# Performance work log

Hardware: AMD Instinct MI355X
Metric: run time of the kernel (lower is better)

Reference implementation:

```python
import jax, jax.numpy as jnp
import numpy as np

MAX_BITS = 256.0  # 2**8


def _quantize_kernel(kern):
    # ConfigurableDense.quantize(): symmetric 8-bit fake-quantization of the kernel.
    # qmin starts at 1e10, qmax at -1e10, so first call uses min/max of kernel.
    qmin = jnp.minimum(jnp.float32(1e10), jnp.min(kern))
    qmax = jnp.maximum(jnp.float32(-1e10), jnp.max(kern))
    s = 2.0 * jnp.maximum(jnp.abs(qmin), jnp.abs(qmax)) / MAX_BITS
    return jnp.round(kern / s) * s


def setup_inputs() -> dict:
    key = jax.random.key(0)
    ks = jax.random.split(key, 9)
    B, S, D_IN, D_MODEL = 4, 2048, 1024, 1024
    sc = 0.02
    return {
        "q": jax.random.normal(ks[0], (B, S, D_IN), jnp.float32),
        "k": jax.random.normal(ks[1], (B, S, D_IN), jnp.float32),
        "v": jax.random.normal(ks[2], (B, S, D_IN), jnp.float32),
        "Wq": jax.random.normal(ks[3], (D_IN, D_MODEL), jnp.float32) * sc,
        "bq": jax.random.normal(ks[4], (D_MODEL,), jnp.float32) * sc,
        "Wk": jax.random.normal(ks[5], (D_IN, D_MODEL), jnp.float32) * sc,
        "bk": jax.random.normal(ks[6], (D_MODEL,), jnp.float32) * sc,
        "Wv": jax.random.normal(ks[7], (D_IN, D_MODEL), jnp.float32) * sc,
        "bv": jax.random.normal(ks[8], (D_MODEL,), jnp.float32) * sc,
    }


def reference(q, k, v, Wq, bq, Wk, bk, Wv, bv):
    # Projections with fake-quantized kernels (ConfigurableDense, activation=None).
    qp = jnp.einsum('bsi,id->bsd', q, _quantize_kernel(Wq)) + bq
    kp = jnp.einsum('bsi,id->bsd', k, _quantize_kernel(Wk)) + bk
    vp = jnp.einsum('bsi,id->bsd', v, _quantize_kernel(Wv)) + bv
    # MovingAverageQuantizers are identity on the first call (steps=0 < warmup).
    dk = jnp.float32(kp.shape[-1])
    logits = jnp.einsum('bqd,bkd->bqk', qp, kp) / jnp.sqrt(dk)  # [B, S, S]
    attn = jax.nn.softmax(logits, axis=-1)
    return jnp.einsum('bqk,bkd->bqd', attn, vp)
```

## Files before the change

kernel.cpp:

```cpp
#include <hip/hip_runtime.h>
#include <stdint.h>


typedef unsigned short ushort_t;
typedef __attribute__((ext_vector_type(8))) short short8;
typedef __bf16 bf16x8 __attribute__((ext_vector_type(8)));
typedef __attribute__((ext_vector_type(4))) float floatx4;
typedef __attribute__((ext_vector_type(8))) int int8v;

__device__ __forceinline__ ushort_t f2bf(float x) {
  unsigned u = __float_as_uint(x);
  unsigned r = (u + 0x7fffu + ((u >> 16) & 1u)) >> 16;
  return (ushort_t)r;
}
__device__ __forceinline__ float bf2f(ushort_t u) {
  return __uint_as_float(((unsigned)u) << 16);
}
__device__ __forceinline__ unsigned char f2fp8(float x) {
  return (unsigned char)(__builtin_amdgcn_cvt_pk_fp8_f32(x, x, 0, false) & 0xff);
}
__device__ __forceinline__ int cvtpk_bf16(float a, float b) {
  unsigned r;
  asm("v_cvt_pk_bf16_f32 %0, %1, %2" : "=v"(r) : "v"(a), "v"(b));
  return (int)r;
}

__device__ __forceinline__ void gl_lds16(const void* g, void* l) {
  __builtin_amdgcn_global_load_lds(
      (const __attribute__((address_space(1))) unsigned int*)g,
      (__attribute__((address_space(3))) unsigned int*)l, 16, 0, 0);
}

__global__ __launch_bounds__(256, 2) void proj_f32a(
    const float* __restrict__ Aq, const float* __restrict__ Ak,
    const float* __restrict__ Av, const ushort_t* __restrict__ Bt,
    void* __restrict__ Cv, void* __restrict__ Cv8,
    const float* __restrict__ bias0, const float* __restrict__ bias1,
    const float* __restrict__ bias2) {
  __shared__ __attribute__((aligned(16))) ushort_t sA[128 * 64];
  __shared__ __attribute__((aligned(16))) ushort_t sB[128 * 64];

  const int t = threadIdx.x;
  const int lane = t & 63;
  const int wave = t >> 6;
  const int bm = blockIdx.x;
  const int bn = blockIdx.y;
  const int bz = blockIdx.z;

  const float* Ab = bz == 0 ? Aq : (bz == 1 ? Ak : Av);
  const ushort_t* Bb = Bt + (long)bz * 1048576L;

  const long a_row0 = (long)bm * 128;
  const long b_row0 = (long)bn * 128;

  const int crow = t >> 3;
  const int schunk = (t & 7) ^ (crow & 7);
  const ushort_t* gB = Bb + (b_row0 + crow) * 1024 + schunk * 8;
  ushort_t* lB = sB + wave * 512;

  const int arow = t >> 3;
  const int achk = t & 7;
  const float* gA = Ab + (a_row0 + arow) * 1024 + achk * 8;
  int awr[4];
#pragma unroll
  for (int k = 0; k < 4; ++k)
    awr[k] = (k * 32 + arow) * 64 + ((achk ^ (arow & 7)) * 8);

  floatx4 acc[4][4];
#pragma unroll
  for (int i = 0; i < 4; ++i)
#pragma unroll
    for (int j = 0; j < 4; ++j) acc[i][j] = {0.f, 0.f, 0.f, 0.f};

  const int wm = (wave & 1) * 64;
  const int wn = (wave >> 1) * 64;
  const int fr = lane & 15;
  const int fg = lane >> 4;

  int offA[2][4], offB[2][4];
#pragma unroll
  for (int s = 0; s < 2; ++s)
#pragma unroll
    for (int i = 0; i < 4; ++i) {
      int rowA = wm + i * 16 + fr;
      int rowB = wn + i * 16 + fr;
      int cg = s * 4 + fg;
      offA[s][i] = rowA * 64 + ((cg ^ (rowA & 7)) * 8);
      offB[s][i] = rowB * 64 + ((cg ^ (rowB & 7)) * 8);
    }

  float4 aL[8];
#pragma unroll
  for (int k = 0; k < 4; ++k) {
    aL[2 * k] = *(const float4*)(gA + (long)k * 32 * 1024);
    aL[2 * k + 1] = *(const float4*)(gA + (long)k * 32 * 1024 + 4);
  }

#pragma unroll 1
  for (int k0 = 0; k0 < 1024; k0 += 64) {
#pragma unroll
    for (int k = 0; k < 4; ++k) {
      int4 w;
      w.x = cvtpk_bf16(aL[2 * k].x, aL[2 * k].y);
      w.y = cvtpk_bf16(aL[2 * k].z, aL[2 * k].w);
      w.z = cvtpk_bf16(aL[2 * k + 1].x, aL[2 * k + 1].y);
      w.w = cvtpk_bf16(aL[2 * k + 1].z, aL[2 * k + 1].w);
      *(int4*)&sA[awr[k]] = w;
    }
#pragma unroll
    for (int i = 0; i < 4; ++i)
      gl_lds16(gB + (long)i * 32 * 1024 + k0, lB + i * 2048);
    __builtin_amdgcn_sched_barrier(0);
    {
      const long kn = (k0 + 64) & 1023;
#pragma unroll
      for (int k = 0; k < 4; ++k) {
        aL[2 * k] = *(const float4*)(gA + (long)k * 32 * 1024 + kn);
        aL[2 * k + 1] = *(const float4*)(gA + (long)k * 32 * 1024 + kn + 4);
      }
    }
    asm volatile("s_waitcnt lgkmcnt(0) vmcnt(8)" ::: "memory");
    __builtin_amdgcn_sched_barrier(0);
    __builtin_amdgcn_s_barrier();
    __builtin_amdgcn_sched_barrier(0);

#pragma unroll
    for (int s = 0; s < 2; ++s) {
      bf16x8 af[4], bfr[4];
#pragma unroll
      for (int i = 0; i < 4; ++i) {
        af[i] = *(const bf16x8*)&sA[offA[s][i]];
        bfr[i] = *(const bf16x8*)&sB[offB[s][i]];
      }
#pragma unroll
      for (int mi = 0; mi < 4; ++mi)
#pragma unroll
        for (int ni = 0; ni < 4; ++ni)
          acc[mi][ni] = __builtin_amdgcn_mfma_f32_16x16x32_bf16(
              af[mi], bfr[ni], acc[mi][ni], 0, 0, 0);
    }
    __builtin_amdgcn_sched_barrier(0);
    __builtin_amdgcn_s_barrier();
    __builtin_amdgcn_sched_barrier(0);
  }

  const int r0 = fg * 4;
  const int cc = fr;
  const float* bias = bz == 0 ? bias0 : (bz == 1 ? bias1 : bias2);
  unsigned char* C8 = (unsigned char*)Cv8 + (long)bz * 8388608L;
  ushort_t* CvpT = (ushort_t*)Cv;

#pragma unroll
  for (int mi = 0; mi < 4; ++mi) {
#pragma unroll
    for (int ni = 0; ni < 4; ++ni) {
      long gm0 = a_row0 + wm + mi * 16 + r0;
      long gn = b_row0 + wn + ni * 16 + cc;
      float vv[4];
#pragma unroll
      for (int r = 0; r < 4; ++r) vv[r] = acc[mi][ni][r] + bias[gn];
      if (bz == 2) {
        long b = gm0 >> 11, s = gm0 & 2047;
        ushort4 u4;
        u4.x = f2bf(vv[0]);
        u4.y = f2bf(vv[1]);
        u4.z = f2bf(vv[2]);
        u4.w = f2bf(vv[3]);
        *(ushort4*)&CvpT[b * (2048L * 1024L) + gn * 2048L + s] = u4;
      } else {
#pragma unroll
        for (int r = 0; r < 4; ++r) C8[(gm0 + r) * 1024 + gn] = f2fp8(vv[r]);
      }
    }
  }
}

#define BM 128
#define BN 128
#define BK 64

template <int CMODE, int SWAP>
__global__ __launch_bounds__(256, 2) void gemm_bt(
    const ushort_t* __restrict__ A, const ushort_t* __restrict__ Bt,
    void* __restrict__ Cv, void* __restrict__ Cv8,
    const float* __restrict__ bias0, const float* __restrict__ bias1,
    const float* __restrict__ bias2, int K, int ldc, float alpha, long strideA,
    long strideB, long strideC) {
  __shared__ __attribute__((aligned(16))) ushort_t sA[BM * BK];
  __shared__ __attribute__((aligned(16))) ushort_t sB[BN * BK];

  const int t = threadIdx.x;
  const int lane = t & 63;
  const int wave = t >> 6;
  const int bm = SWAP ? blockIdx.x : blockIdx.y;
  const int bn = SWAP ? blockIdx.y : blockIdx.x;
  const int bz = blockIdx.z;

  const ushort_t* Ab = A + (long)bz * strideA;
  const ushort_t* Bb = Bt + (long)bz * strideB;

  const long a_row0 = (long)bm * BM;
  const long b_row0 = (long)bn * BN;

  const int crow = t >> 3;
  const int schunk = (t & 7) ^ (crow & 7);

  const ushort_t* gA = Ab + (a_row0 + crow) * (long)K + schunk * 8;
  const ushort_t* gB = Bb + (b_row0 + crow) * (long)K + schunk * 8;

  ushort_t* lA = sA + wave * 512;
  ushort_t* lB = sB + wave * 512;

  floatx4 acc[4][4];
#pragma unroll
  for (int i = 0; i < 4; ++i)
#pragma unroll
    for (int j = 0; j < 4; ++j) acc[i][j] = {0.f, 0.f, 0.f, 0.f};

  const int wm = (wave & 1) * 64;
  const int wn = (wave >> 1) * 64;
  const int fr = lane & 15;
  const int fg = lane >> 4;

  int offA[2][4], offB[2][4];
#pragma unroll
  for (int s = 0; s < 2; ++s)
#pragma unroll
    for (int i = 0; i < 4; ++i) {
      int rowA = wm + i * 16 + fr;
      int rowB = wn + i * 16 + fr;
      int cg = s * 4 + fg;
      offA[s][i] = rowA * BK + ((cg ^ (rowA & 7)) * 8);
      offB[s][i] = rowB * BK + ((cg ^ (rowB & 7)) * 8);
    }

  for (int k0 = 0; k0 < K; k0 += BK) {
#pragma unroll
    for (int i = 0; i < 4; ++i) {
      gl_lds16(gA + (long)i * 32 * K, lA + i * 2048);
      gl_lds16(gB + (long)i * 32 * K, lB + i * 2048);
    }
    gA += BK;
    gB += BK;
    __syncthreads();

#pragma unroll
    for (int s = 0; s < 2; ++s) {
      bf16x8 af[4], bfr[4];
#pragma unroll
      for (int i = 0; i < 4; ++i) {
        af[i] = *(const bf16x8*)&sA[offA[s][i]];
        bfr[i] = *(const bf16x8*)&sB[offB[s][i]];
      }
#pragma unroll
      for (int mi = 0; mi < 4; ++mi)
#pragma unroll
        for (int ni = 0; ni < 4; ++ni)
          acc[mi][ni] = __builtin_amdgcn_mfma_f32_16x16x32_bf16(
              af[mi], bfr[ni], acc[mi][ni], 0, 0, 0);
    }
    __syncthreads();
  }

  const int r0 = fg * 4;
  const int cc = fr;
  float* Cz32 = (float*)Cv + (long)bz * strideC;

#pragma unroll
  for (int mi = 0; mi < 4; ++mi) {
#pragma unroll
    for (int ni = 0; ni < 4; ++ni) {
      long gm0 = a_row0 + wm + mi * 16 + r0;
      long gn = b_row0 + wn + ni * 16 + cc;
      float vv[4];
#pragma unroll
      for (int r = 0; r < 4; ++r) vv[r] = acc[mi][ni][r] * alpha;
      if (CMODE == 2) {
#pragma unroll
        for (int r = 0; r < 4; ++r) Cz32[(gm0 + r) * ldc + gn] = vv[r];
      }
    }
  }
}

__global__ __launch_bounds__(256, 2) void qk_fp8(
    const unsigned char* __restrict__ Q8, const unsigned char* __restrict__ K8,
    ushort_t* __restrict__ P) {
  __shared__ __attribute__((aligned(16))) unsigned char sA[128 * 128];
  __shared__ __attribute__((aligned(16))) unsigned char sB[128 * 128];
  const int t = threadIdx.x;
  const int lane = t & 63, wave = t >> 6;
  const int bm = blockIdx.x, bn = blockIdx.y, bz = blockIdx.z;

  const unsigned char* Ab = Q8 + (long)bz * 2097152L + (long)bm * 128 * 1024;
  const unsigned char* Bb = K8 + (long)bz * 2097152L + (long)bn * 128 * 1024;

  const int crow = t >> 3;
  const int schunk = (t & 7) ^ (crow & 7);
  const unsigned char* gA = Ab + crow * 1024 + schunk * 16;
  const unsigned char* gB = Bb + crow * 1024 + schunk * 16;
  unsigned char* lA = sA + wave * 1024;
  unsigned char* lB = sB + wave * 1024;

  floatx4 acc[4][4];
#pragma unroll
  for (int i = 0; i < 4; ++i)
#pragma unroll
    for (int j = 0; j < 4; ++j) acc[i][j] = {0.f, 0.f, 0.f, 0.f};

  const int wm = (wave & 1) * 64;
  const int wn = (wave >> 1) * 64;
  const int fr = lane & 15;
  const int fg = lane >> 4;

  int offA[4][2], offB[4][2];
#pragma unroll
  for (int i = 0; i < 4; ++i) {
    int rA = wm + i * 16 + fr;
    int rB = wn + i * 16 + fr;
    offA[i][0] = rA * 128 + (((2 * fg) ^ (rA & 7)) * 16);
    offA[i][1] = rA * 128 + (((2 * fg + 1) ^ (rA & 7)) * 16);
    offB[i][0] = rB * 128 + (((2 * fg) ^ (rB & 7)) * 16);
    offB[i][1] = rB * 128 + (((2 * fg + 1) ^ (rB & 7)) * 16);
  }

  for (int k0 = 0; k0 < 1024; k0 += 128) {
#pragma unroll
    for (int i = 0; i < 4; ++i) {
      gl_lds16(gA + (long)i * 32 * 1024, lA + i * 4096);
      gl_lds16(gB + (long)i * 32 * 1024, lB + i * 4096);
    }
    gA += 128;
    gB += 128;
    __syncthreads();

    int8v af[4], bfr[4];
#pragma unroll
    for (int i = 0; i < 4; ++i) {
      int4 lo = *(const int4*)&sA[offA[i][0]];
      int4 hi = *(const int4*)&sA[offA[i][1]];
      af[i][0] = lo.x; af[i][1] = lo.y; af[i][2] = lo.z; af[i][3] = lo.w;
      af[i][4] = hi.x; af[i][5] = hi.y; af[i][6] = hi.z; af[i][7] = hi.w;
      int4 lo2 = *(const int4*)&sB[offB[i][0]];
      int4 hi2 = *(const int4*)&sB[offB[i][1]];
      bfr[i][0] = lo2.x; bfr[i][1] = lo2.y; bfr[i][2] = lo2.z; bfr[i][3] = lo2.w;
      bfr[i][4] = hi2.x; bfr[i][5] = hi2.y; bfr[i][6] = hi2.z; bfr[i][7] = hi2.w;
    }
#pragma unroll
    for (int mi = 0; mi < 4; ++mi)
#pragma unroll
      for (int ni = 0; ni < 4; ++ni)
        acc[mi][ni] = __builtin_amdgcn_mfma_scale_f32_16x16x128_f8f6f4(
            af[mi], bfr[ni], acc[mi][ni], 0, 0, 0, 127, 0, 127);
    __syncthreads();
  }

  const int r0 = fg * 4;
  const int cc = fr;
#pragma unroll
  for (int mi = 0; mi < 4; ++mi)
#pragma unroll
    for (int ni = 0; ni < 4; ++ni)
#pragma unroll
      for (int r = 0; r < 4; ++r) {
        long gm = (long)bm * 128 + wm + mi * 16 + r0 + r;
        long gn = (long)bn * 128 + wn + ni * 16 + cc;
        P[(long)bz * 4194304L + gm * 2048 + gn] =
            f2bf(acc[mi][ni][r] * 0.03125f);
      }
}

__global__ __launch_bounds__(256) void absmax_k(
    const float* __restrict__ W0, const float* __restrict__ W1,
    const float* __restrict__ W2, unsigned* __restrict__ outv) {
  const float* W = blockIdx.z == 0 ? W0 : (blockIdx.z == 1 ? W1 : W2);
  float m = 0.f;
  const long n = 1024L * 1024L;
  for (long i = (long)blockIdx.x * blockDim.x + threadIdx.x; i < n;
       i += (long)gridDim.x * blockDim.x)
    m = fmaxf(m, fabsf(W[i]));
  for (int off = 32; off; off >>= 1) m = fmaxf(m, __shfl_xor(m, off));
  __shared__ float red[4];
  int lane = threadIdx.x & 63, wave = threadIdx.x >> 6;
  if (lane == 0) red[wave] = m;
  __syncthreads();
  if (threadIdx.x == 0) {
    m = fmaxf(fmaxf(red[0], red[1]), fmaxf(red[2], red[3]));
    atomicMax(&outv[blockIdx.z], __float_as_uint(m));
  }
}

__global__ __launch_bounds__(256) void quant_w_k(
    const float* __restrict__ W0, const float* __restrict__ W1,
    const float* __restrict__ W2, const unsigned* __restrict__ scales,
    ushort_t* __restrict__ Wt) {
  const int z = blockIdx.z;
  const float* W = z == 0 ? W0 : (z == 1 ? W1 : W2);
  const float s = __uint_as_float(scales[z]) * (1.0f / 128.0f);
  __shared__ float tile[32][33];
  const int tx = threadIdx.x & 31, ty = threadIdx.x >> 5;
  const int k0 = blockIdx.y * 32, n0 = blockIdx.x * 32;
#pragma unroll
  for (int i = 0; i < 4; ++i)
    tile[ty + i * 8][tx] = W[(long)(k0 + ty + i * 8) * 1024 + n0 + tx];
  __syncthreads();
  ushort_t* wt = Wt + (long)z * 1024 * 1024;
#pragma unroll
  for (int i = 0; i < 4; ++i) {
    float w = tile[tx][ty + i * 8];
    float qv = rintf(w / s) * s;
    wt[(long)(n0 + ty + i * 8) * 1024 + k0 + tx] = f2bf(qv);
  }
}

__global__ __launch_bounds__(256) void softmax_k(ushort_t* __restrict__ P) {
  const long row = blockIdx.x;
  ushort_t* p = P + row * 2048;
  const int t = threadIdx.x;
  const int lane = t & 63, wave = t >> 6;
  short8 v8 = *(const short8*)&p[t * 8];
  float x[8];
#pragma unroll
  for (int j = 0; j < 8; ++j) x[j] = bf2f((ushort_t)v8[j]);
  float m = x[0];
#pragma unroll
  for (int j = 1; j < 8; ++j) m = fmaxf(m, x[j]);
  for (int off = 32; off; off >>= 1) m = fmaxf(m, __shfl_xor(m, off));
  __shared__ float rmax[4], rsum[4];
  if (lane == 0) rmax[wave] = m;
  __syncthreads();
  m = fmaxf(fmaxf(rmax[0], rmax[1]), fmaxf(rmax[2], rmax[3]));
  float s = 0.f;
#pragma unroll
  for (int j = 0; j < 8; ++j) {
    x[j] = __expf(x[j] - m);
    s += x[j];
  }
  for (int off = 32; off; off >>= 1) s += __shfl_xor(s, off);
  if (lane == 0) rsum[wave] = s;
  __syncthreads();
  s = rsum[0] + rsum[1] + rsum[2] + rsum[3];
  float inv = 1.0f / s;
  short8 o8;
#pragma unroll
  for (int j = 0; j < 8; ++j) o8[j] = (short)f2bf(x[j] * inv);
  *(short8*)&p[t * 8] = o8;
}

extern "C" void kernel_launch(void* const* d_in, const int* in_sizes, int n_in,
                              void* d_out, int out_size, void* d_ws,
                              size_t ws_size, hipStream_t stream) {
  const float* q = (const float*)d_in[0];
  const float* k = (const float*)d_in[1];
  const float* v = (const float*)d_in[2];
  const float* Wq = (const float*)d_in[3];
  const float* bq = (const float*)d_in[4];
  const float* Wk = (const float*)d_in[5];
  const float* bk = (const float*)d_in[6];
  const float* Wv = (const float*)d_in[7];
  const float* bv = (const float*)d_in[8];
  float* out = (float*)d_out;
  char* ws = (char*)d_ws;

  unsigned* scales = (unsigned*)ws;
  ushort_t* Wt = (ushort_t*)(ws + 256);
  ushort_t* P = (ushort_t*)(ws + 6291712);
  ushort_t* vpT = (ushort_t*)(ws + 73400576);
  unsigned char* qp8 = (unsigned char*)(ws + 90177792);
  unsigned char* kp8 = (unsigned char*)(ws + 98566400);

  hipMemsetAsync(scales, 0, 64, stream);
  absmax_k<<<dim3(64, 1, 3), 256, 0, stream>>>(Wq, Wk, Wv, scales);
  quant_w_k<<<dim3(32, 32, 3), 256, 0, stream>>>(Wq, Wk, Wv, scales, Wt);

  proj_f32a<<<dim3(64, 8, 3), 256, 0, stream>>>(q, k, v, Wt, vpT, qp8, bq, bk,
                                                bv);

  qk_fp8<<<dim3(16, 16, 4), 256, 0, stream>>>(qp8, kp8, P);

  softmax_k<<<8192, 256, 0, stream>>>(P);

  gemm_bt<2, 1><<<dim3(16, 8, 4), 256, 0, stream>>>(
      P, vpT, out, nullptr, nullptr, nullptr, nullptr, 2048, 1024, 1.0f,
      4194304L, 2097152L, 2097152L);
}
```

Measured before the change: 310.8 us.

## Double-buffer B tile in projection GEMM and ping-pong A register prefetch

The projection GEMM's K loop is restructured with a double-buffered shared-memory B tile and two alternating register sets for the fp32 A tile. The B async load for the next step is issued a full iteration ahead, and the loop is unrolled by two with explicit prologue and epilogue. The aim is to hide global-to-LDS latency behind MFMA work. In exchange it uses more LDS (16KB extra per block) and more VGPRs, which could lower occupancy under launch_bounds(256,2).

```diff
diff --git a/kernel.cpp b/kernel.cpp
--- a/kernel.cpp
+++ b/kernel.cpp
@@ -30,6 +30,75 @@
       (const __attribute__((address_space(1))) unsigned int*)g,
       (__attribute__((address_space(3))) unsigned int*)l, 16, 0, 0);
 }
+
+
+#define SB0() __builtin_amdgcn_sched_barrier(0)
+
+#define LOAD_A(dst, kt)                                                \
+  {                                                                    \
+    const long kb = (long)((kt) & 15) * 64;                            \
+    _Pragma("unroll") for (int k = 0; k < 4; ++k) {                    \
+      dst[2 * k] = *(const float4*)(gA + (long)k * 32 * 1024 + kb);    \
+      dst[2 * k + 1] =                                                 \
+          *(const float4*)(gA + (long)k * 32 * 1024 + kb + 4);         \
+    }                                                                  \
+  }
+#define CVTWR(src)                                                     \
+  {                                                                    \
+    _Pragma("unroll") for (int k = 0; k < 4; ++k) {                    \
+      int4 w;                                                          \
+      w.x = cvtpk_bf16(src[2 * k].x, src[2 * k].y);                    \
+      w.y = cvtpk_bf16(src[2 * k].z, src[2 * k].w);                    \
+      w.z = cvtpk_bf16(src[2 * k + 1].x, src[2 * k + 1].y);            \
+      w.w = cvtpk_bf16(src[2 * k + 1].z, src[2 * k + 1].w);            \
+      *(int4*)&sA[awr[k]] = w;                                         \
+    }                                                                  \
+  }
+#define STB(kt, buf)                                                   \
+  {                                                                    \
+    _Pragma("unroll") for (int i = 0; i < 4; ++i)                      \
+        gl_lds16(gB + (long)i * 32 * 1024 + (long)((kt) & 15) * 64,    \
+                 lB + (buf)*8192 + i * 2048);                          \
+  }
+#define COMPUTE(CB)                                                          \
+  {                                                                          \
+    _Pragma("unroll") for (int s = 0; s < 2; ++s) {                          \
+      bf16x8 af[4], bfr[4];                                                  \
+      _Pragma("unroll") for (int i = 0; i < 4; ++i) {                        \
+        af[i] = *(const bf16x8*)&sA[offA[s][i]];                             \
+        bfr[i] = *(const bf16x8*)&sB[(CB)*8192 + offB[s][i]];                \
+      }                                                                      \
+      _Pragma("unroll") for (int mi = 0; mi < 4; ++mi)                       \
+          _Pragma("unroll") for (int ni = 0; ni < 4; ++ni) acc[mi][ni] =     \
+              __builtin_amdgcn_mfma_f32_16x16x32_bf16(af[mi], bfr[ni],       \
+                                                      acc[mi][ni], 0, 0, 0); \
+    }                                                                        \
+  }
+#define PRE_BARRIER()                                   \
+  {                                                     \
+    asm volatile("s_waitcnt lgkmcnt(0)" ::: "memory");  \
+    SB0();                                              \
+    __builtin_amdgcn_s_barrier();                       \
+    SB0();                                              \
+  }
+#define END_BARRIER()                                             \
+  {                                                               \
+    asm volatile("s_waitcnt lgkmcnt(0) vmcnt(8)" ::: "memory");   \
+    SB0();                                                        \
+    __builtin_amdgcn_s_barrier();                                 \
+    SB0();                                                        \
+  }
+#define ITER(t, AC, AN)          \
+  {                              \
+    STB((t) + 1, ((t) + 1) & 1); \
+    CVTWR(AC);                   \
+    SB0();                       \
+    LOAD_A(AN, (t) + 1);         \
+    SB0();                       \
+    PRE_BARRIER();               \
+    COMPUTE((t)&1);              \
+    END_BARRIER();               \
+  }
 
 __global__ __launch_bounds__(256, 2) void proj_f32a(
     const float* __restrict__ Aq, const float* __restrict__ Ak,
@@ -38,7 +107,7 @@
     const float* __restrict__ bias0, const float* __restrict__ bias1,
     const float* __restrict__ bias2) {
   __shared__ __attribute__((aligned(16))) ushort_t sA[128 * 64];
-  __shared__ __attribute__((aligned(16))) ushort_t sB[128 * 64];
+  __shared__ __attribute__((aligned(16))) ushort_t sB[2 * 128 * 64];
 
   const int t = threadIdx.x;
   const int lane = t & 63;
@@ -89,60 +158,33 @@
       offB[s][i] = rowB * 64 + ((cg ^ (rowB & 7)) * 8);
     }
 
-  float4 aL[8];
-#pragma unroll
-  for (int k = 0; k < 4; ++k) {
-    aL[2 * k] = *(const float4*)(gA + (long)k * 32 * 1024);
-    aL[2 * k + 1] = *(const float4*)(gA + (long)k * 32 * 1024 + 4);
-  }
+  float4 aX[8], aY[8];
+
+  LOAD_A(aX, 0);
+  STB(0, 0);
+  STB(1, 1);
+  CVTWR(aX);
+  SB0();
+  LOAD_A(aY, 1);
+  SB0();
+  asm volatile("s_waitcnt lgkmcnt(0) vmcnt(12)" ::: "memory");
+  SB0();
+  __builtin_amdgcn_s_barrier();
+  SB0();
+  COMPUTE(0);
+  END_BARRIER();
 
 #pragma unroll 1
-  for (int k0 = 0; k0 < 1024; k0 += 64) {
-#pragma unroll
-    for (int k = 0; k < 4; ++k) {
-      int4 w;
-      w.x = cvtpk_bf16(aL[2 * k].x, aL[2 * k].y);
-      w.y = cvtpk_bf16(aL[2 * k].z, aL[2 * k].w);
-      w.z = cvtpk_bf16(aL[2 * k + 1].x, aL[2 * k + 1].y);
-      w.w = cvtpk_bf16(aL[2 * k + 1].z, aL[2 * k + 1].w);
-      *(int4*)&sA[awr[k]] = w;
-    }
-#pragma unroll
-    for (int i = 0; i < 4; ++i)
-      gl_lds16(gB + (long)i * 32 * 1024 + k0, lB + i * 2048);
-    __builtin_amdgcn_sched_barrier(0);
-    {
-      const long kn = (k0 + 64) & 1023;
-#pragma unroll
-      for (int k = 0; k < 4; ++k) {
-        aL[2 * k] = *(const float4*)(gA + (long)k * 32 * 1024 + kn);
-        aL[2 * k + 1] = *(const float4*)(gA + (long)k * 32 * 1024 + kn + 4);
-      }
-    }
-    asm volatile("s_waitcnt lgkmcnt(0) vmcnt(8)" ::: "memory");
-    __builtin_amdgcn_sched_barrier(0);
-    __builtin_amdgcn_s_barrier();
-    __builtin_amdgcn_sched_barrier(0);
-
-#pragma unroll
-    for (int s = 0; s < 2; ++s) {
-      bf16x8 af[4], bfr[4];
-#pragma unroll
-      for (int i = 0; i < 4; ++i) {
-        af[i] = *(const bf16x8*)&sA[offA[s][i]];
-        bfr[i] = *(const bf16x8*)&sB[offB[s][i]];
-      }
-#pragma unroll
-      for (int mi = 0; mi < 4; ++mi)
-#pragma unroll
-        for (int ni = 0; ni < 4; ++ni)
-          acc[mi][ni] = __builtin_amdgcn_mfma_f32_16x16x32_bf16(
-              af[mi], bfr[ni], acc[mi][ni], 0, 0, 0);
-    }
-    __builtin_amdgcn_sched_barrier(0);
-    __builtin_amdgcn_s_barrier();
-    __builtin_amdgcn_sched_barrier(0);
-  }
+  for (int tp = 0; tp < 7; ++tp) {
+    const int t1 = 2 * tp + 1;
+    ITER(t1, aY, aX);
+    ITER(t1 + 1, aX, aY);
+  }
+
+  CVTWR(aY);
+  SB0();
+  PRE_BARRIER();
+  COMPUTE(1);
 
   const int r0 = fg * 4;
   const int cc = fr;
```

New measurement: 307.8 us. Within noise of the previous version (-0.9%).

## Load fp32 activations directly to LDS and convert to bf16 at fragment read

Applied to the files above, without the earlier changes.

The projection GEMM no longer loads fp32 activations into registers, converts them to bf16 and stores them to LDS. It now streams fp32 A tiles straight into LDS with global_load_lds, using an XOR swizzle, and converts to bf16 when reading MFMA fragments. This frees VGPRs and removes the register staging path, but it doubles the LDS footprint for A and repeats the conversion for every wave that reads a fragment. It also drops the software prefetch of the next A tile and replaces the fine-grained waitcnt and barrier scheduling with plain __syncthreads, so load latency is no longer overlapped with compute.

```diff
diff --git a/kernel.cpp b/kernel.cpp
--- a/kernel.cpp
+++ b/kernel.cpp
@@ -37,7 +37,7 @@
     void* __restrict__ Cv, void* __restrict__ Cv8,
     const float* __restrict__ bias0, const float* __restrict__ bias1,
     const float* __restrict__ bias2) {
-  __shared__ __attribute__((aligned(16))) ushort_t sA[128 * 64];
+  __shared__ __attribute__((aligned(16))) float sAf[128 * 64];
   __shared__ __attribute__((aligned(16))) ushort_t sB[128 * 64];
 
   const int t = threadIdx.x;
@@ -53,18 +53,15 @@
   const long a_row0 = (long)bm * 128;
   const long b_row0 = (long)bn * 128;
 
-  const int crow = t >> 3;
-  const int schunk = (t & 7) ^ (crow & 7);
-  const ushort_t* gB = Bb + (b_row0 + crow) * 1024 + schunk * 8;
+  const int brow = t >> 3;
+  const int schB = (t & 7) ^ (brow & 7);
+  const ushort_t* gB = Bb + (b_row0 + brow) * 1024 + schB * 8;
   ushort_t* lB = sB + wave * 512;
 
-  const int arow = t >> 3;
-  const int achk = t & 7;
-  const float* gA = Ab + (a_row0 + arow) * 1024 + achk * 8;
-  int awr[4];
-#pragma unroll
-  for (int k = 0; k < 4; ++k)
-    awr[k] = (k * 32 + arow) * 64 + ((achk ^ (arow & 7)) * 8);
+  const int arow = t >> 4;
+  const int schA = (t & 15) ^ arow;
+  const float* gA = Ab + (a_row0 + arow) * 1024 + schA * 4;
+  float* lA = sAf + wave * 256;
 
   floatx4 acc[4][4];
 #pragma unroll
@@ -77,59 +74,43 @@
   const int fr = lane & 15;
   const int fg = lane >> 4;
 
-  int offA[2][4], offB[2][4];
+  int offAf[2][4][2], offB[2][4];
 #pragma unroll
   for (int s = 0; s < 2; ++s)
 #pragma unroll
     for (int i = 0; i < 4; ++i) {
       int rowA = wm + i * 16 + fr;
+      int c0 = s * 8 + fg * 2;
+      offAf[s][i][0] = rowA * 64 + ((c0 ^ fr) * 4);
+      offAf[s][i][1] = rowA * 64 + (((c0 + 1) ^ fr) * 4);
       int rowB = wn + i * 16 + fr;
       int cg = s * 4 + fg;
-      offA[s][i] = rowA * 64 + ((cg ^ (rowA & 7)) * 8);
       offB[s][i] = rowB * 64 + ((cg ^ (rowB & 7)) * 8);
     }
-
-  float4 aL[8];
-#pragma unroll
-  for (int k = 0; k < 4; ++k) {
-    aL[2 * k] = *(const float4*)(gA + (long)k * 32 * 1024);
-    aL[2 * k + 1] = *(const float4*)(gA + (long)k * 32 * 1024 + 4);
-  }
 
 #pragma unroll 1
   for (int k0 = 0; k0 < 1024; k0 += 64) {
 #pragma unroll
-    for (int k = 0; k < 4; ++k) {
-      int4 w;
-      w.x = cvtpk_bf16(aL[2 * k].x, aL[2 * k].y);
-      w.y = cvtpk_bf16(aL[2 * k].z, aL[2 * k].w);
-      w.z = cvtpk_bf16(aL[2 * k + 1].x, aL[2 * k + 1].y);
-      w.w = cvtpk_bf16(aL[2 * k + 1].z, aL[2 * k + 1].w);
-      *(int4*)&sA[awr[k]] = w;
-    }
+    for (int i = 0; i < 8; ++i)
+      gl_lds16(gA + (long)i * 16 * 1024 + k0, lA + i * 1024);
 #pragma unroll
     for (int i = 0; i < 4; ++i)
       gl_lds16(gB + (long)i * 32 * 1024 + k0, lB + i * 2048);
-    __builtin_amdgcn_sched_barrier(0);
-    {
-      const long kn = (k0 + 64) & 1023;
-#pragma unroll
-      for (int k = 0; k < 4; ++k) {
-        aL[2 * k] = *(const float4*)(gA + (long)k * 32 * 1024 + kn);
-        aL[2 * k + 1] = *(const float4*)(gA + (long)k * 32 * 1024 + kn + 4);
-      }
-    }
-    asm volatile("s_waitcnt lgkmcnt(0) vmcnt(8)" ::: "memory");
-    __builtin_amdgcn_sched_barrier(0);
-    __builtin_amdgcn_s_barrier();
-    __builtin_amdgcn_sched_barrier(0);
+    __syncthreads();
 
 #pragma unroll
     for (int s = 0; s < 2; ++s) {
       bf16x8 af[4], bfr[4];
 #pragma unroll
       for (int i = 0; i < 4; ++i) {
-        af[i] = *(const bf16x8*)&sA[offA[s][i]];
+        float4 lo = *(const float4*)&sAf[offAf[s][i][0]];
+        float4 hi = *(const float4*)&sAf[offAf[s][i][1]];
+        int4 w;
+        w.x = cvtpk_bf16(lo.x, lo.y);
+        w.y = cvtpk_bf16(lo.z, lo.w);
+        w.z = cvtpk_bf16(hi.x, hi.y);
+        w.w = cvtpk_bf16(hi.z, hi.w);
+        af[i] = *(const bf16x8*)&w;
         bfr[i] = *(const bf16x8*)&sB[offB[s][i]];
       }
 #pragma unroll
@@ -139,9 +120,7 @@
           acc[mi][ni] = __builtin_amdgcn_mfma_f32_16x16x32_bf16(
               af[mi], bfr[ni], acc[mi][ni], 0, 0, 0);
     }
-    __builtin_amdgcn_sched_barrier(0);
-    __builtin_amdgcn_s_barrier();
-    __builtin_amdgcn_sched_barrier(0);
+    __syncthreads();
   }
 
   const int r0 = fg * 4;
```

Result: no change. 309.4 us (-0.4%).
